# Optimization experiments

Measured on AMD Instinct MI355X. Metric: run time of the kernel, lower is better.

The kernel has to match this reference:

```python
import jax, jax.numpy as jnp
import numpy as np

B, S, D_IN, D_HID, STEPS = 64, 512, 1024, 1024, 64


def setup_inputs() -> dict:
    key = jax.random.key(0)
    ks = jax.random.split(key, 8)
    w = 0.02
    return {
        "hx": jax.random.normal(ks[0], (B, D_HID), jnp.float32),
        "cx": jax.random.normal(ks[1], (B, D_HID), jnp.float32),
        "ctx": jax.random.normal(ks[2], (B, S, D_IN), jnp.float32),
        "ctx_mask": jnp.ones((B, S), jnp.float32),
        "Wh": jax.random.normal(ks[3], (4 * D_HID, D_HID), jnp.float32) * w,
        "bh": jnp.zeros((4 * D_HID,), jnp.float32),
        "W_in": jax.random.normal(ks[4], (D_IN, D_HID), jnp.float32) * w,
        "W_out": jax.random.normal(ks[5], (D_HID, 2 * D_IN), jnp.float32) * w,
        "steps": STEPS,
    }


def _attention(hy, ctx, ctx_mask, W_in, W_out):
    # hy: [B, D_HID] -> inp: [B, D_IN]
    inp = hy @ W_in.T
    attn = jnp.einsum("bsd,bd->bs", ctx, inp) - (1.0 - ctx_mask) * 100000.0
    attn = jax.nn.softmax(attn, axis=-1)
    weighted_ctx = jnp.einsum("bs,bsd->bd", attn, ctx)
    h_tilde = jnp.tanh(jnp.concatenate([weighted_ctx, inp], axis=1) @ W_out.T)
    return h_tilde


def reference(hx, cx, ctx, ctx_mask, Wh, bh, W_in, W_out, steps):
    def step(carry, _):
        h, c = carry
        gates = h @ Wh.T + bh
        i, f, g, o = jnp.split(gates, 4, axis=1)
        cy = jax.nn.sigmoid(f) * c + jax.nn.sigmoid(i) * jnp.tanh(g)
        hy = jax.nn.sigmoid(o) * jnp.tanh(cy)
        h_tilde = _attention(hy, ctx, ctx_mask, W_in, W_out)
        return (h_tilde, cy), h_tilde

    (hx, cx), outs = jax.lax.scan(step, (hx, cx), None, length=steps)
    # outs: [steps, B, D_HID] -> batch_first [B, steps, D_HID]
    output = jnp.transpose(outs, (1, 0, 2))
    return output, hx, cx
```

## Files before the change

### kernel.cpp

```cpp
#include <hip/hip_runtime.h>
#include <hip/hip_bf16.h>


#define B_    64
#define S_    512
#define DHID  1024
#define STEPS 64

__device__ __forceinline__ float sigmf(float x) { return 1.0f / (1.0f + expf(-x)); }

__global__ __launch_bounds__(256) void gemm64_part(
    const float* __restrict__ A, int lda,
    const float* __restrict__ B, int ldb,
    float* __restrict__ Cp, int N, int kchunk) {
  __shared__ __align__(16) float As[64][20];
  __shared__ __align__(16) float Bs[64][20];
  const int tid = threadIdx.x;
  const int tx = tid & 15, ty = tid >> 4;
  const int n0 = blockIdx.x * 64;
  const int kc = blockIdx.y;
  float acc[4][4] = {};
  const int kbeg = kc * kchunk, kend = kbeg + kchunk;
  for (int k0 = kbeg; k0 < kend; k0 += 16) {
    __syncthreads();
#pragma unroll
    for (int p = 0; p < 4; ++p) {
      As[p * 16 + ty][tx] = A[(size_t)(p * 16 + ty) * lda + k0 + tx];
      Bs[p * 16 + ty][tx] = B[(size_t)(n0 + p * 16 + ty) * ldb + k0 + tx];
    }
    __syncthreads();
#pragma unroll
    for (int kk = 0; kk < 16; kk += 4) {
      float4 av[4], bv[4];
#pragma unroll
      for (int i = 0; i < 4; ++i) av[i] = *(const float4*)&As[ty * 4 + i][kk];
#pragma unroll
      for (int j = 0; j < 4; ++j) bv[j] = *(const float4*)&Bs[tx * 4 + j][kk];
#pragma unroll
      for (int i = 0; i < 4; ++i)
#pragma unroll
        for (int j = 0; j < 4; ++j)
          acc[i][j] += av[i].x * bv[j].x + av[i].y * bv[j].y +
                       av[i].z * bv[j].z + av[i].w * bv[j].w;
    }
  }
  float* Cpart = Cp + (size_t)kc * 64 * N;
#pragma unroll
  for (int i = 0; i < 4; ++i)
#pragma unroll
    for (int j = 0; j < 4; ++j)
      Cpart[(size_t)(ty * 4 + i) * N + n0 + tx * 4 + j] = acc[i][j];
}

__global__ __launch_bounds__(256) void cell_k(
    const float* __restrict__ gatesP, const float* __restrict__ bh,
    float* __restrict__ c, float* __restrict__ hy) {
  int idx = blockIdx.x * 256 + threadIdx.x;
  int b = idx >> 10, j = idx & 1023;
  float gi = bh[j], gf = bh[1024 + j], gg = bh[2048 + j], go = bh[3072 + j];
#pragma unroll
  for (int p = 0; p < 4; ++p) {
    const float* gp = gatesP + (size_t)p * 64 * 4096 + (size_t)b * 4096;
    gi += gp[j]; gf += gp[1024 + j]; gg += gp[2048 + j]; go += gp[3072 + j];
  }
  float cy = sigmf(gf) * c[idx] + sigmf(gi) * tanhf(gg);
  c[idx] = cy;
  hy[idx] = sigmf(go) * tanhf(cy);
}

__global__ __launch_bounds__(256) void attn_k(
    const float* __restrict__ ctx, const float* __restrict__ mask,
    const float* __restrict__ inpP,
    float* __restrict__ pm, float* __restrict__ pl, float* __restrict__ pw) {
  const int b = blockIdx.x, ch = blockIdx.y;
  const int tid = threadIdx.x;
  const int lane = tid & 63, w = tid >> 6;
  __shared__ __align__(16) float inp_s[1024];
  __shared__ __align__(16) float ctx_s[16][1024];
  __shared__ float sc_s[16];
  for (int i = tid; i < 1024; i += 256) {
    float v = 0.f;
#pragma unroll
    for (int p = 0; p < 8; ++p) v += inpP[(size_t)p * 65536 + (size_t)b * 1024 + i];
    inp_s[i] = v;
  }
  float m = -1e30f, l = 0.f;
  float pwv[4] = {0.f, 0.f, 0.f, 0.f};
  const float4* base = (const float4*)(ctx + (size_t)b * S_ * 1024 + (size_t)ch * 128 * 1024);
  for (int st = 0; st < 8; ++st) {
    __syncthreads();
    const float4* src = base + (size_t)st * 4096;
    float4* dst = (float4*)ctx_s;
    for (int i = tid; i < 4096; i += 256) dst[i] = src[i];
    __syncthreads();
    for (int ss = w; ss < 16; ss += 4) {
      const float* row = ctx_s[ss];
      float p = 0.f;
#pragma unroll
      for (int i = 0; i < 16; ++i) p += row[lane + 64 * i] * inp_s[lane + 64 * i];
#pragma unroll
      for (int off = 32; off; off >>= 1) p += __shfl_down(p, off, 64);
      if (lane == 0) {
        float mk = mask[b * S_ + ch * 128 + st * 16 + ss];
        sc_s[ss] = p - (1.0f - mk) * 100000.0f;
      }
    }
    __syncthreads();
    float mloc = m;
#pragma unroll
    for (int ss = 0; ss < 16; ++ss) mloc = fmaxf(mloc, sc_s[ss]);
    float r = __expf(m - mloc);
    l *= r;
#pragma unroll
    for (int i = 0; i < 4; ++i) pwv[i] *= r;
    float e[16];
#pragma unroll
    for (int ss = 0; ss < 16; ++ss) { e[ss] = __expf(sc_s[ss] - mloc); l += e[ss]; }
#pragma unroll
    for (int i = 0; i < 4; ++i) {
      int d = tid + 256 * i;
      float a = 0.f;
#pragma unroll
      for (int ss = 0; ss < 16; ++ss) a += e[ss] * ctx_s[ss][d];
      pwv[i] += a;
    }
    m = mloc;
  }
  const int part = b * 4 + ch;
  if (tid == 0) { pm[part] = m; pl[part] = l; }
#pragma unroll
  for (int i = 0; i < 4; ++i) pw[(size_t)part * 1024 + tid + 256 * i] = pwv[i];
}

__global__ __launch_bounds__(256) void merge_k(
    const float* __restrict__ pm, const float* __restrict__ pl,
    const float* __restrict__ pw, const float* __restrict__ inpP,
    float* __restrict__ cat) {
  int idx = blockIdx.x * 256 + threadIdx.x;
  int b = idx >> 10, d = idx & 1023;
  float m0 = pm[b * 4 + 0], m1 = pm[b * 4 + 1], m2 = pm[b * 4 + 2], m3 = pm[b * 4 + 3];
  float M = fmaxf(fmaxf(m0, m1), fmaxf(m2, m3));
  float w0 = __expf(m0 - M), w1 = __expf(m1 - M), w2 = __expf(m2 - M), w3 = __expf(m3 - M);
  float denom = w0 * pl[b * 4 + 0] + w1 * pl[b * 4 + 1] + w2 * pl[b * 4 + 2] + w3 * pl[b * 4 + 3];
  float acc = w0 * pw[(size_t)(b * 4 + 0) * 1024 + d] + w1 * pw[(size_t)(b * 4 + 1) * 1024 + d] +
              w2 * pw[(size_t)(b * 4 + 2) * 1024 + d] + w3 * pw[(size_t)(b * 4 + 3) * 1024 + d];
  cat[(size_t)b * 2048 + d] = acc / denom;
  float v = 0.f;
#pragma unroll
  for (int p = 0; p < 8; ++p) v += inpP[(size_t)p * 65536 + idx];
  cat[(size_t)b * 2048 + 1024 + d] = v;
}

__global__ __launch_bounds__(256) void final_k(
    const float* __restrict__ hpreP, const float* __restrict__ c,
    float* __restrict__ h, float* __restrict__ out, int t) {
  int idx = blockIdx.x * 256 + threadIdx.x;
  int b = idx >> 10, j = idx & 1023;
  float s = 0.f;
#pragma unroll
  for (int p = 0; p < 16; ++p) s += hpreP[(size_t)p * 65536 + idx];
  float ht = tanhf(s);
  out[((size_t)b * STEPS + t) * 1024 + j] = ht;
  h[idx] = ht;
  if (t == STEPS - 1) {
    out[(size_t)B_ * STEPS * 1024 + idx] = ht;
    out[(size_t)B_ * STEPS * 1024 + 65536 + idx] = c[idx];
  }
}

__global__ __launch_bounds__(256) void init_k(
    const float* __restrict__ hx, const float* __restrict__ cx,
    float* __restrict__ h, float* __restrict__ c) {
  int idx = blockIdx.x * 256 + threadIdx.x;
  h[idx] = hx[idx];
  c[idx] = cx[idx];
}

extern "C" void kernel_launch(void* const* d_in, const int* in_sizes, int n_in,
                              void* d_out, int out_size, void* d_ws, size_t ws_size,
                              hipStream_t stream) {
  const float* hx   = (const float*)d_in[0];
  const float* cx   = (const float*)d_in[1];
  const float* ctx  = (const float*)d_in[2];
  const float* mask = (const float*)d_in[3];
  const float* Wh   = (const float*)d_in[4];
  const float* bh   = (const float*)d_in[5];
  const float* Win  = (const float*)d_in[6];
  const float* Wout = (const float*)d_in[7];
  float* out = (float*)d_out;

  float* ws = (float*)d_ws;
  float* h      = ws;
  float* c      = h + 65536;
  float* hy     = c + 65536;
  float* gatesP = hy + 65536;
  float* inpP   = gatesP + 4 * 262144;
  float* cat    = inpP + 8 * 65536;
  float* hpreP  = cat + 131072;
  float* pm     = hpreP + 16 * 65536;
  float* pl     = pm + 256;
  float* pw     = pl + 256;

  init_k<<<256, 256, 0, stream>>>(hx, cx, h, c);
  for (int t = 0; t < STEPS; ++t) {
    gemm64_part<<<dim3(64, 4), 256, 0, stream>>>(h, 1024, Wh, 1024, gatesP, 4096, 256);
    cell_k<<<256, 256, 0, stream>>>(gatesP, bh, c, hy);
    gemm64_part<<<dim3(16, 8), 256, 0, stream>>>(hy, 1024, Win, 1024, inpP, 1024, 128);
    attn_k<<<dim3(64, 4), 256, 0, stream>>>(ctx, mask, inpP, pm, pl, pw);
    merge_k<<<256, 256, 0, stream>>>(pm, pl, pw, inpP, cat);
    gemm64_part<<<dim3(16, 16), 256, 0, stream>>>(cat, 2048, Wout, 2048, hpreP, 1024, 128);
    final_k<<<256, 256, 0, stream>>>(hpreP, c, h, out, t);
  }
}
```

Baseline: 7.190 ms.

## Fuse all LSTM-attention steps into one cooperative persistent kernel with grid syncs

```diff
diff --git a/kernel.cpp b/kernel.cpp
--- a/kernel.cpp
+++ b/kernel.cpp
@@ -1,41 +1,48 @@
 #include <hip/hip_runtime.h>
 #include <hip/hip_bf16.h>
-
-
-#define B_    64
-#define S_    512
-#define DHID  1024
+#include <hip/hip_cooperative_groups.h>
+
+namespace cg = cooperative_groups;
+
+
 #define STEPS 64
 
-__device__ __forceinline__ float sigmf(float x) { return 1.0f / (1.0f + expf(-x)); }
-
-__global__ __launch_bounds__(256) void gemm64_part(
-    const float* __restrict__ A, int lda,
-    const float* __restrict__ B, int ldb,
-    float* __restrict__ Cp, int N, int kchunk) {
-  __shared__ __align__(16) float As[64][20];
-  __shared__ __align__(16) float Bs[64][20];
+struct Params {
+  const float *hx, *cx, *ctx, *mask, *Wh, *bh, *Win, *Wout;
+  float *out;
+  float *h, *c, *hy, *gatesP, *inpP, *inpR, *pm, *pl, *pw, *outP;
+};
+
+union __align__(16) Smem {
+  struct { float As[64][20]; float Bs[64][20]; } g;
+  struct { float inp[1024]; float ctx[8][1024]; float sc[8]; } a;
+  struct { float A[64][132]; float Bs[64][20]; float wc[64][4]; } o;
+};
+
+__device__ __forceinline__ float sigmf(float x) { return 1.f / (1.f + __expf(-x)); }
+
+__device__ void gemm_g(const float* __restrict__ A, int lda,
+                       const float* __restrict__ Bm, int ldb,
+                       float* __restrict__ Cp, int N, int n0,
+                       int kbeg, int kend, Smem& s) {
   const int tid = threadIdx.x;
   const int tx = tid & 15, ty = tid >> 4;
-  const int n0 = blockIdx.x * 64;
-  const int kc = blockIdx.y;
   float acc[4][4] = {};
-  const int kbeg = kc * kchunk, kend = kbeg + kchunk;
   for (int k0 = kbeg; k0 < kend; k0 += 16) {
     __syncthreads();
 #pragma unroll
-    for (int p = 0; p < 4; ++p) {
-      As[p * 16 + ty][tx] = A[(size_t)(p * 16 + ty) * lda + k0 + tx];
-      Bs[p * 16 + ty][tx] = B[(size_t)(n0 + p * 16 + ty) * ldb + k0 + tx];
+    for (int q = 0; q < 4; ++q) {
+      s.g.As[q * 16 + ty][tx] = A[(size_t)(q * 16 + ty) * lda + k0 + tx];
+      s.g.Bs[q * 16 + ty][tx] = Bm[(size_t)(n0 + q * 16 + ty) * ldb + k0 + tx];
     }
     __syncthreads();
 #pragma unroll
     for (int kk = 0; kk < 16; kk += 4) {
       float4 av[4], bv[4];
 #pragma unroll
-      for (int i = 0; i < 4; ++i) av[i] = *(const float4*)&As[ty * 4 + i][kk];
-#pragma unroll
-      for (int j = 0; j < 4; ++j) bv[j] = *(const float4*)&Bs[tx * 4 + j][kk];
+      for (int i = 0; i < 4; ++i) av[i] = *(const float4*)&s.g.As[ty * 4 + i][kk];
+#pragma unroll
+      for (int j = 0; j < 4; ++j) bv[j] = *(const float4*)&s.g.Bs[tx * 4 + j][kk];
 #pragma unroll
       for (int i = 0; i < 4; ++i)
 #pragma unroll
@@ -44,171 +51,251 @@
                        av[i].z * bv[j].z + av[i].w * bv[j].w;
     }
   }
-  float* Cpart = Cp + (size_t)kc * 64 * N;
 #pragma unroll
   for (int i = 0; i < 4; ++i)
 #pragma unroll
     for (int j = 0; j < 4; ++j)
-      Cpart[(size_t)(ty * 4 + i) * N + n0 + tx * 4 + j] = acc[i][j];
-}
-
-__global__ __launch_bounds__(256) void cell_k(
-    const float* __restrict__ gatesP, const float* __restrict__ bh,
-    float* __restrict__ c, float* __restrict__ hy) {
-  int idx = blockIdx.x * 256 + threadIdx.x;
+      Cp[(size_t)(ty * 4 + i) * N + n0 + tx * 4 + j] = acc[i][j];
+}
+
+__device__ void gemm_o(const float* __restrict__ Bm, int ldb, int kgbeg,
+                       float* __restrict__ Cp, int N, int n0, Smem& s) {
+  const int tid = threadIdx.x;
+  const int tx = tid & 15, ty = tid >> 4;
+  float acc[4][4] = {};
+  for (int k0 = 0; k0 < 128; k0 += 16) {
+    __syncthreads();
+#pragma unroll
+    for (int q = 0; q < 4; ++q)
+      s.o.Bs[q * 16 + ty][tx] = Bm[(size_t)(n0 + q * 16 + ty) * ldb + kgbeg + k0 + tx];
+    __syncthreads();
+#pragma unroll
+    for (int kk = 0; kk < 16; kk += 4) {
+      float4 av[4], bv[4];
+#pragma unroll
+      for (int i = 0; i < 4; ++i) av[i] = *(const float4*)&s.o.A[ty * 4 + i][k0 + kk];
+#pragma unroll
+      for (int j = 0; j < 4; ++j) bv[j] = *(const float4*)&s.o.Bs[tx * 4 + j][kk];
+#pragma unroll
+      for (int i = 0; i < 4; ++i)
+#pragma unroll
+        for (int j = 0; j < 4; ++j)
+          acc[i][j] += av[i].x * bv[j].x + av[i].y * bv[j].y +
+                       av[i].z * bv[j].z + av[i].w * bv[j].w;
+    }
+  }
+#pragma unroll
+  for (int i = 0; i < 4; ++i)
+#pragma unroll
+    for (int j = 0; j < 4; ++j)
+      Cp[(size_t)(ty * 4 + i) * N + n0 + tx * 4 + j] = acc[i][j];
+}
+
+__device__ void phase0(const Params& p, int bid, int tid) {
+  int idx = bid * 256 + tid;
+  p.h[idx] = p.hx[idx];
+  p.c[idx] = p.cx[idx];
+}
+
+__device__ void phase1(const Params& p, int bid, int tid, Smem& s) {
+  int nt = bid >> 2, kc = bid & 3;
+  gemm_g(p.h, 1024, p.Wh, 1024, p.gatesP + (size_t)kc * 262144, 4096,
+         nt * 64, kc * 256, kc * 256 + 256, s);
+}
+
+__device__ void phase2(const Params& p, int bid, int tid) {
+  int idx = bid * 256 + tid;
   int b = idx >> 10, j = idx & 1023;
-  float gi = bh[j], gf = bh[1024 + j], gg = bh[2048 + j], go = bh[3072 + j];
-#pragma unroll
-  for (int p = 0; p < 4; ++p) {
-    const float* gp = gatesP + (size_t)p * 64 * 4096 + (size_t)b * 4096;
+  float gi = p.bh[j], gf = p.bh[1024 + j], gg = p.bh[2048 + j], go = p.bh[3072 + j];
+#pragma unroll
+  for (int q = 0; q < 4; ++q) {
+    const float* gp = p.gatesP + (size_t)q * 262144 + (size_t)b * 4096;
     gi += gp[j]; gf += gp[1024 + j]; gg += gp[2048 + j]; go += gp[3072 + j];
   }
-  float cy = sigmf(gf) * c[idx] + sigmf(gi) * tanhf(gg);
-  c[idx] = cy;
-  hy[idx] = sigmf(go) * tanhf(cy);
-}
-
-__global__ __launch_bounds__(256) void attn_k(
-    const float* __restrict__ ctx, const float* __restrict__ mask,
-    const float* __restrict__ inpP,
-    float* __restrict__ pm, float* __restrict__ pl, float* __restrict__ pw) {
-  const int b = blockIdx.x, ch = blockIdx.y;
-  const int tid = threadIdx.x;
+  float cy = sigmf(gf) * p.c[idx] + sigmf(gi) * tanhf(gg);
+  p.c[idx] = cy;
+  p.hy[idx] = sigmf(go) * tanhf(cy);
+}
+
+__device__ void phase3(const Params& p, int bid, int tid, Smem& s) {
+  int nt = bid >> 4, kc = bid & 15;
+  gemm_g(p.hy, 1024, p.Win, 1024, p.inpP + (size_t)kc * 65536, 1024,
+         nt * 64, kc * 64, kc * 64 + 64, s);
+}
+
+__device__ void phase4(const Params& p, int bid, int tid, Smem& s) {
+  const int b = bid >> 2, ch = bid & 3;
   const int lane = tid & 63, w = tid >> 6;
-  __shared__ __align__(16) float inp_s[1024];
-  __shared__ __align__(16) float ctx_s[16][1024];
-  __shared__ float sc_s[16];
   for (int i = tid; i < 1024; i += 256) {
     float v = 0.f;
 #pragma unroll
-    for (int p = 0; p < 8; ++p) v += inpP[(size_t)p * 65536 + (size_t)b * 1024 + i];
-    inp_s[i] = v;
-  }
+    for (int q = 0; q < 16; ++q) v += p.inpP[(size_t)q * 65536 + (size_t)b * 1024 + i];
+    s.a.inp[i] = v;
+    if (ch == 0) p.inpR[(size_t)b * 1024 + i] = v;
+  }
+  __syncthreads();
+  float inpr[16];
+#pragma unroll
+  for (int i = 0; i < 16; ++i) inpr[i] = s.a.inp[lane + 64 * i];
+
   float m = -1e30f, l = 0.f;
   float pwv[4] = {0.f, 0.f, 0.f, 0.f};
-  const float4* base = (const float4*)(ctx + (size_t)b * S_ * 1024 + (size_t)ch * 128 * 1024);
-  for (int st = 0; st < 8; ++st) {
-    __syncthreads();
-    const float4* src = base + (size_t)st * 4096;
-    float4* dst = (float4*)ctx_s;
-    for (int i = tid; i < 4096; i += 256) dst[i] = src[i];
-    __syncthreads();
-    for (int ss = w; ss < 16; ss += 4) {
-      const float* row = ctx_s[ss];
-      float p = 0.f;
-#pragma unroll
-      for (int i = 0; i < 16; ++i) p += row[lane + 64 * i] * inp_s[lane + 64 * i];
-#pragma unroll
-      for (int off = 32; off; off >>= 1) p += __shfl_down(p, off, 64);
+  const float4* base = (const float4*)(p.ctx + (size_t)b * 524288 + (size_t)ch * 131072);
+  for (int st = 0; st < 16; ++st) {
+    __syncthreads();
+    const float4* src = base + (size_t)st * 2048;
+    float4* dst = (float4*)s.a.ctx;
+    for (int i = tid; i < 2048; i += 256) dst[i] = src[i];
+    __syncthreads();
+    for (int ss = w; ss < 8; ss += 4) {
+      const float* row = s.a.ctx[ss];
+      float acc = 0.f;
+#pragma unroll
+      for (int i = 0; i < 16; ++i) acc += row[lane + 64 * i] * inpr[i];
+#pragma unroll
+      for (int off = 32; off; off >>= 1) acc += __shfl_down(acc, off, 64);
       if (lane == 0) {
-        float mk = mask[b * S_ + ch * 128 + st * 16 + ss];
-        sc_s[ss] = p - (1.0f - mk) * 100000.0f;
+        float mk = p.mask[b * 512 + ch * 128 + st * 8 + ss];
+        s.a.sc[ss] = acc - (1.f - mk) * 100000.f;
       }
     }
     __syncthreads();
     float mloc = m;
 #pragma unroll
-    for (int ss = 0; ss < 16; ++ss) mloc = fmaxf(mloc, sc_s[ss]);
+    for (int ss = 0; ss < 8; ++ss) mloc = fmaxf(mloc, s.a.sc[ss]);
     float r = __expf(m - mloc);
     l *= r;
 #pragma unroll
     for (int i = 0; i < 4; ++i) pwv[i] *= r;
-    float e[16];
-#pragma unroll
-    for (int ss = 0; ss < 16; ++ss) { e[ss] = __expf(sc_s[ss] - mloc); l += e[ss]; }
+    float e[8];
+#pragma unroll
+    for (int ss = 0; ss < 8; ++ss) { e[ss] = __expf(s.a.sc[ss] - mloc); l += e[ss]; }
 #pragma unroll
     for (int i = 0; i < 4; ++i) {
       int d = tid + 256 * i;
-      float a = 0.f;
-#pragma unroll
-      for (int ss = 0; ss < 16; ++ss) a += e[ss] * ctx_s[ss][d];
-      pwv[i] += a;
+      float a2 = 0.f;
+#pragma unroll
+      for (int ss = 0; ss < 8; ++ss) a2 += e[ss] * s.a.ctx[ss][d];
+      pwv[i] += a2;
     }
     m = mloc;
   }
-  const int part = b * 4 + ch;
-  if (tid == 0) { pm[part] = m; pl[part] = l; }
-#pragma unroll
-  for (int i = 0; i < 4; ++i) pw[(size_t)part * 1024 + tid + 256 * i] = pwv[i];
-}
-
-__global__ __launch_bounds__(256) void merge_k(
-    const float* __restrict__ pm, const float* __restrict__ pl,
-    const float* __restrict__ pw, const float* __restrict__ inpP,
-    float* __restrict__ cat) {
-  int idx = blockIdx.x * 256 + threadIdx.x;
-  int b = idx >> 10, d = idx & 1023;
-  float m0 = pm[b * 4 + 0], m1 = pm[b * 4 + 1], m2 = pm[b * 4 + 2], m3 = pm[b * 4 + 3];
-  float M = fmaxf(fmaxf(m0, m1), fmaxf(m2, m3));
-  float w0 = __expf(m0 - M), w1 = __expf(m1 - M), w2 = __expf(m2 - M), w3 = __expf(m3 - M);
-  float denom = w0 * pl[b * 4 + 0] + w1 * pl[b * 4 + 1] + w2 * pl[b * 4 + 2] + w3 * pl[b * 4 + 3];
-  float acc = w0 * pw[(size_t)(b * 4 + 0) * 1024 + d] + w1 * pw[(size_t)(b * 4 + 1) * 1024 + d] +
-              w2 * pw[(size_t)(b * 4 + 2) * 1024 + d] + w3 * pw[(size_t)(b * 4 + 3) * 1024 + d];
-  cat[(size_t)b * 2048 + d] = acc / denom;
+  int part = b * 4 + ch;
+  if (tid == 0) { p.pm[part] = m; p.pl[part] = l; }
+#pragma unroll
+  for (int i = 0; i < 4; ++i) p.pw[(size_t)part * 1024 + tid + 256 * i] = pwv[i];
+}
+
+__device__ void phase5(const Params& p, int bid, int tid, Smem& s) {
+  const int nt = bid >> 4, kc = bid & 15, n0 = nt * 64;
+  if (kc < 8) {
+    if (tid < 64) {
+      int b = tid;
+      float m0 = p.pm[b * 4], m1 = p.pm[b * 4 + 1], m2 = p.pm[b * 4 + 2], m3 = p.pm[b * 4 + 3];
+      float M = fmaxf(fmaxf(m0, m1), fmaxf(m2, m3));
+      float w0 = __expf(m0 - M), w1 = __expf(m1 - M), w2 = __expf(m2 - M), w3 = __expf(m3 - M);
+      float inv = 1.f / (w0 * p.pl[b * 4] + w1 * p.pl[b * 4 + 1] +
+                         w2 * p.pl[b * 4 + 2] + w3 * p.pl[b * 4 + 3]);
+      s.o.wc[b][0] = w0 * inv; s.o.wc[b][1] = w1 * inv;
+      s.o.wc[b][2] = w2 * inv; s.o.wc[b][3] = w3 * inv;
+    }
+    __syncthreads();
+    for (int e = tid; e < 8192; e += 256) {
+      int b = e >> 7, d = e & 127, col = kc * 128 + d;
+      float v = s.o.wc[b][0] * p.pw[(size_t)(b * 4 + 0) * 1024 + col] +
+                s.o.wc[b][1] * p.pw[(size_t)(b * 4 + 1) * 1024 + col] +
+                s.o.wc[b][2] * p.pw[(size_t)(b * 4 + 2) * 1024 + col] +
+                s.o.wc[b][3] * p.pw[(size_t)(b * 4 + 3) * 1024 + col];
+      s.o.A[b][d] = v;
+    }
+  } else {
+    for (int e = tid; e < 8192; e += 256) {
+      int b = e >> 7, d = e & 127;
+      s.o.A[b][d] = p.inpR[(size_t)b * 1024 + (kc - 8) * 128 + d];
+    }
+  }
+  __syncthreads();
+  gemm_o(p.Wout, 2048, kc * 128, p.outP + (size_t)kc * 65536, 1024, n0, s);
+}
+
+__device__ void phase6(const Params& p, int bid, int tid, int t) {
+  int idx = bid * 256 + tid;
   float v = 0.f;
 #pragma unroll
-  for (int p = 0; p < 8; ++p) v += inpP[(size_t)p * 65536 + idx];
-  cat[(size_t)b * 2048 + 1024 + d] = v;
-}
-
-__global__ __launch_bounds__(256) void final_k(
-    const float* __restrict__ hpreP, const float* __restrict__ c,
-    float* __restrict__ h, float* __restrict__ out, int t) {
-  int idx = blockIdx.x * 256 + threadIdx.x;
+  for (int q = 0; q < 16; ++q) v += p.outP[(size_t)q * 65536 + idx];
+  float ht = tanhf(v);
   int b = idx >> 10, j = idx & 1023;
-  float s = 0.f;
-#pragma unroll
-  for (int p = 0; p < 16; ++p) s += hpreP[(size_t)p * 65536 + idx];
-  float ht = tanhf(s);
-  out[((size_t)b * STEPS + t) * 1024 + j] = ht;
-  h[idx] = ht;
+  p.out[((size_t)b * STEPS + t) * 1024 + j] = ht;
+  p.h[idx] = ht;
   if (t == STEPS - 1) {
-    out[(size_t)B_ * STEPS * 1024 + idx] = ht;
-    out[(size_t)B_ * STEPS * 1024 + 65536 + idx] = c[idx];
-  }
-}
-
-__global__ __launch_bounds__(256) void init_k(
-    const float* __restrict__ hx, const float* __restrict__ cx,
-    float* __restrict__ h, float* __restrict__ c) {
-  int idx = blockIdx.x * 256 + threadIdx.x;
-  h[idx] = hx[idx];
-  c[idx] = cx[idx];
-}
+    p.out[(size_t)4194304 + idx] = ht;
+    p.out[(size_t)4194304 + 65536 + idx] = p.c[idx];
+  }
+}
+
+__global__ __launch_bounds__(256, 1) void fused_k(Params p) {
+  __shared__ Smem s;
+  cg::grid_group grid = cg::this_grid();
+  const int bid = blockIdx.x, tid = threadIdx.x;
+  phase0(p, bid, tid);
+  grid.sync();
+  for (int t = 0; t < STEPS; ++t) {
+    phase1(p, bid, tid, s); grid.sync();
+    phase2(p, bid, tid);    grid.sync();
+    phase3(p, bid, tid, s); grid.sync();
+    phase4(p, bid, tid, s); grid.sync();
+    phase5(p, bid, tid, s); grid.sync();
+    phase6(p, bid, tid, t); grid.sync();
+  }
+}
+
+__global__ __launch_bounds__(256) void p0_k(Params p) { phase0(p, blockIdx.x, threadIdx.x); }
+__global__ __launch_bounds__(256) void p1_k(Params p) { __shared__ Smem s; phase1(p, blockIdx.x, threadIdx.x, s); }
+__global__ __launch_bounds__(256) void p2_k(Params p) { phase2(p, blockIdx.x, threadIdx.x); }
+__global__ __launch_bounds__(256) void p3_k(Params p) { __shared__ Smem s; phase3(p, blockIdx.x, threadIdx.x, s); }
+__global__ __launch_bounds__(256) void p4_k(Params p) { __shared__ Smem s; phase4(p, blockIdx.x, threadIdx.x, s); }
+__global__ __launch_bounds__(256) void p5_k(Params p) { __shared__ Smem s; phase5(p, blockIdx.x, threadIdx.x, s); }
+__global__ __launch_bounds__(256) void p6_k(Params p, int t) { phase6(p, blockIdx.x, threadIdx.x, t); }
 
 extern "C" void kernel_launch(void* const* d_in, const int* in_sizes, int n_in,
                               void* d_out, int out_size, void* d_ws, size_t ws_size,
                               hipStream_t stream) {
-  const float* hx   = (const float*)d_in[0];
-  const float* cx   = (const float*)d_in[1];
-  const float* ctx  = (const float*)d_in[2];
-  const float* mask = (const float*)d_in[3];
-  const float* Wh   = (const float*)d_in[4];
-  const float* bh   = (const float*)d_in[5];
-  const float* Win  = (const float*)d_in[6];
-  const float* Wout = (const float*)d_in[7];
-  float* out = (float*)d_out;
+  Params prm;
+  prm.hx   = (const float*)d_in[0];
+  prm.cx   = (const float*)d_in[1];
+  prm.ctx  = (const float*)d_in[2];
+  prm.mask = (const float*)d_in[3];
+  prm.Wh   = (const float*)d_in[4];
+  prm.bh   = (const float*)d_in[5];
+  prm.Win  = (const float*)d_in[6];
+  prm.Wout = (const float*)d_in[7];
+  prm.out  = (float*)d_out;
 
   float* ws = (float*)d_ws;
-  float* h      = ws;
-  float* c      = h + 65536;
-  float* hy     = c + 65536;
-  float* gatesP = hy + 65536;
-  float* inpP   = gatesP + 4 * 262144;
-  float* cat    = inpP + 8 * 65536;
-  float* hpreP  = cat + 131072;
-  float* pm     = hpreP + 16 * 65536;
-  float* pl     = pm + 256;
-  float* pw     = pl + 256;
-
-  init_k<<<256, 256, 0, stream>>>(hx, cx, h, c);
-  for (int t = 0; t < STEPS; ++t) {
-    gemm64_part<<<dim3(64, 4), 256, 0, stream>>>(h, 1024, Wh, 1024, gatesP, 4096, 256);
-    cell_k<<<256, 256, 0, stream>>>(gatesP, bh, c, hy);
-    gemm64_part<<<dim3(16, 8), 256, 0, stream>>>(hy, 1024, Win, 1024, inpP, 1024, 128);
-    attn_k<<<dim3(64, 4), 256, 0, stream>>>(ctx, mask, inpP, pm, pl, pw);
-    merge_k<<<256, 256, 0, stream>>>(pm, pl, pw, inpP, cat);
-    gemm64_part<<<dim3(16, 16), 256, 0, stream>>>(cat, 2048, Wout, 2048, hpreP, 1024, 128);
-    final_k<<<256, 256, 0, stream>>>(hpreP, c, h, out, t);
-  }
-}
+  prm.h      = ws; ws += 65536;
+  prm.c      = ws; ws += 65536;
+  prm.hy     = ws; ws += 65536;
+  prm.gatesP = ws; ws += 4 * 262144;
+  prm.inpP   = ws; ws += 16 * 65536;
+  prm.inpR   = ws; ws += 65536;
+  prm.pm     = ws; ws += 256;
+  prm.pl     = ws; ws += 256;
+  prm.pw     = ws; ws += 262144;
+  prm.outP   = ws; ws += 16 * 65536;
+
+  void* args[] = { &prm };
+  hipError_t err = hipLaunchCooperativeKernel((const void*)fused_k, dim3(256), dim3(256),
+                                              args, 0, stream);
+  if (err != hipSuccess) {
+    (void)hipGetLastError();
+    p0_k<<<256, 256, 0, stream>>>(prm);
+    for (int t = 0; t < STEPS; ++t) {
+      p1_k<<<256, 256, 0, stream>>>(prm);
+      p2_k<<<256, 256, 0, stream>>>(prm);
+      p3_k<<<256, 256, 0, stream>>>(prm);
+      p4_k<<<256, 256, 0, stream>>>(prm);
+      p5_k<<<256, 256, 0, stream>>>(prm);
+      p6_k<<<256, 256, 0, stream>>>(prm, t);
+    }
+  }
+}
```

New measurement: 19.20 ms. 167% more time.
